# Kernel optimization log

Measured on AMD Instinct MI355X. Metric: run time of the kernel, lower is better.

Reference implementation:

```python
import jax, jax.numpy as jnp
import numpy as np

B, L, D, H = 2, 2048, 1024, 16
HD = D // H

def setup_inputs() -> dict:
    key = jax.random.key(0)
    ks = jax.random.split(key, 9)
    s = 1.0 / np.sqrt(D)
    return {
        "x": jax.random.normal(ks[0], (B, L, D), jnp.float32),
        "Wq": jax.random.normal(ks[1], (D, D), jnp.float32) * s,
        "bq": jax.random.normal(ks[2], (D,), jnp.float32) * 0.02,
        "Wk": jax.random.normal(ks[3], (D, D), jnp.float32) * s,
        "bk": jax.random.normal(ks[4], (D,), jnp.float32) * 0.02,
        "Wv": jax.random.normal(ks[5], (D, D), jnp.float32) * s,
        "bv": jax.random.normal(ks[6], (D,), jnp.float32) * 0.02,
        "Wo": jax.random.normal(ks[7], (D, D), jnp.float32) * s,
        "bo": jax.random.normal(ks[8], (D,), jnp.float32) * 0.02,
    }

def reference(x, Wq, bq, Wk, bk, Wv, bv, Wo, bo):
    b, l, d = x.shape
    # projections -> [B, H, L, HD]
    def split_heads(t):
        return t.reshape(b, l, H, HD).transpose(0, 2, 1, 3)
    Q = split_heads(x @ Wq + bq)
    K = split_heads(x @ Wk + bk)
    V = split_heads(x @ Wv + bv)
    scores = jnp.einsum('bhqd,bhkd->bhqk', Q, K)  # [B,H,L,L]
    causal = jnp.tril(jnp.ones((l, l), bool))
    scores = jnp.where(causal, scores, -jnp.inf)
    attn = jax.nn.softmax(scores / np.sqrt(HD), axis=-1)
    ctx = jnp.einsum('bhqk,bhkd->bhqd', attn, V)
    ctx = ctx.transpose(0, 2, 1, 3).reshape(b, l, d)
    return ctx @ Wo + bo
```

## Files before the change

### kernel.cpp

```cpp
#include <hip/hip_runtime.h>
#include <stdint.h>

typedef unsigned short u16;
typedef __attribute__((ext_vector_type(8))) __bf16 bf16x8;
typedef __attribute__((ext_vector_type(4))) float f32x4;
typedef __attribute__((ext_vector_type(16))) float f32x16;

#define BM 128
#define BN 128
#define BK 32

__device__ __forceinline__ u16 f2bf(float f) {
  union { float f; uint32_t u; } c; c.f = f;
  uint32_t u = c.u + 0x7fffu + ((c.u >> 16) & 1u);
  return (u16)(u >> 16);
}
__device__ __forceinline__ uint32_t cvtpk(float a, float b) {
  uint32_t r;
  asm("v_cvt_pk_bf16_f32 %0, %1, %2" : "=v"(r) : "v"(a), "v"(b));
  return r;
}

__device__ __forceinline__ void async16(const u16* g, u16* l) {
  __builtin_amdgcn_global_load_lds(
      (const __attribute__((address_space(1))) void*)g,
      (__attribute__((address_space(3))) void*)l, 16, 0, 0);
}

__device__ __forceinline__ f32x4 mfma16(bf16x8 a, bf16x8 b, f32x4 c) {
  return __builtin_amdgcn_mfma_f32_16x16x32_bf16(a, b, c, 0, 0, 0);
}
__device__ __forceinline__ f32x16 mfma32(bf16x8 a, bf16x8 b, f32x16 c) {
  return __builtin_amdgcn_mfma_f32_32x32x16_bf16(a, b, c, 0, 0, 0);
}


__global__ __launch_bounds__(256) void x_cvt_kernel(const float* __restrict__ x,
                                                    u16* __restrict__ xb) {
  int i = (blockIdx.x * 256 + threadIdx.x) * 4;
  float4 v = *(const float4*)(x + i);
  uint2 t; t.x = cvtpk(v.x, v.y); t.y = cvtpk(v.z, v.w);
  *(uint2*)(xb + i) = t;
}

__global__ __launch_bounds__(256) void wt_cvt_kernel(const float* __restrict__ Wq,
                                                     const float* __restrict__ Wk,
                                                     const float* __restrict__ Wv,
                                                     const float* __restrict__ Wo,
                                                     u16* __restrict__ out) {
  __shared__ __align__(16) u16 t[64][72];
  int z = blockIdx.z;
  const float* W = (z == 0) ? Wq : (z == 1) ? Wk : (z == 2) ? Wv : Wo;
  u16* o = out + (size_t)z * (1u << 20);
  int n0 = blockIdx.x * 64, k0 = blockIdx.y * 64;
  int tid = threadIdx.x;
  int c4 = (tid & 15) * 4, r0 = tid >> 4;
#pragma unroll
  for (int i = 0; i < 4; i++) {
    int r = r0 + i * 16;
    float4 v = *(const float4*)(W + (size_t)(k0 + r) * 1024 + n0 + c4);
    t[c4 + 0][r] = f2bf(v.x);
    t[c4 + 1][r] = f2bf(v.y);
    t[c4 + 2][r] = f2bf(v.z);
    t[c4 + 3][r] = f2bf(v.w);
  }
  __syncthreads();
  int n = tid >> 2, kc = (tid & 3) * 16;
  uint4 a = *(const uint4*)&t[n][kc];
  uint4 b = *(const uint4*)&t[n][kc + 8];
  *(uint4*)(o + (size_t)(n0 + n) * 1024 + k0 + kc) = a;
  *(uint4*)(o + (size_t)(n0 + n) * 1024 + k0 + kc + 8) = b;
}


__device__ __forceinline__ void gemm_core(const u16* __restrict__ A,
                                          const u16* __restrict__ Bt,
                                          u16* As, u16* Bs, f32x4 (&acc)[4][4]) {
  const int tid = threadIdx.x, wave = tid >> 6, lane = tid & 63;
  const int low = lane & 15, hi = lane >> 4;
  const int wm = wave >> 1, wn = wave & 1;
  const int m0 = blockIdx.y * BM, n0 = blockIdx.x * BN;
  const f32x4 fzero = {0.f, 0.f, 0.f, 0.f};
#pragma unroll
  for (int i = 0; i < 4; i++)
#pragma unroll
    for (int j = 0; j < 4; j++) acc[i][j] = fzero;

  const u16* ap = As + (wm * 64 + low) * BK + hi * 8;
  const u16* bp = Bs + (wn * 64 + low) * BK + hi * 8;

  const int e0 = wave * 128 + lane;
  const int e1 = e0 + 64;
  const u16* ga0 = A + (size_t)(m0 + (e0 >> 2)) * 1024 + (e0 & 3) * 8;
  const u16* ga1 = A + (size_t)(m0 + (e1 >> 2)) * 1024 + (e1 & 3) * 8;
  const u16* gb0 = Bt + (size_t)(n0 + (e0 >> 2)) * 1024 + (e0 & 3) * 8;
  const u16* gb1 = Bt + (size_t)(n0 + (e1 >> 2)) * 1024 + (e1 & 3) * 8;
  u16* la0 = As + (wave * 2 + 0) * 512;
  u16* la1 = As + (wave * 2 + 1) * 512;
  u16* lb0 = Bs + (wave * 2 + 0) * 512;
  u16* lb1 = Bs + (wave * 2 + 1) * 512;

  for (int kt = 0; kt < 1024; kt += BK) {
    __syncthreads();
    async16(ga0 + kt, la0);
    async16(ga1 + kt, la1);
    async16(gb0 + kt, lb0);
    async16(gb1 + kt, lb1);
    __syncthreads();
    bf16x8 af[4], bfv[4];
#pragma unroll
    for (int i = 0; i < 4; i++) af[i] = *(const bf16x8*)(ap + i * 16 * BK);
#pragma unroll
    for (int j = 0; j < 4; j++) bfv[j] = *(const bf16x8*)(bp + j * 16 * BK);
#pragma unroll
    for (int i = 0; i < 4; i++)
#pragma unroll
      for (int j = 0; j < 4; j++) acc[i][j] = mfma16(af[i], bfv[j], acc[i][j]);
  }
}

__global__ __launch_bounds__(256) void gemm_qkv_kernel(
    const u16* __restrict__ xb, const u16* __restrict__ wT,
    const float* __restrict__ bq, const float* __restrict__ bk,
    const float* __restrict__ bv,
    u16* __restrict__ qs, u16* __restrict__ ks, u16* __restrict__ vts) {
  __shared__ __align__(16) u16 As[BM * BK];
  __shared__ __align__(16) u16 Bs[BN * BK];
  const int z = blockIdx.z;
  const u16* Bt = wT + (size_t)z * (1u << 20);
  f32x4 acc[4][4];
  gemm_core(xb, Bt, As, Bs, acc);

  const float* bias = (z == 0) ? bq : (z == 1) ? bk : bv;
  u16* out = (z == 0) ? qs : (z == 1) ? ks : vts;
  const float scale = (z == 0) ? 0.180336880f : 1.0f;
  const int tid = threadIdx.x, wave = tid >> 6, lane = tid & 63;
  const int low = lane & 15, hi = lane >> 4;
  const int wm = wave >> 1, wn = wave & 1;
  const int m0 = blockIdx.y * BM, n0 = blockIdx.x * BN;
#pragma unroll
  for (int i = 0; i < 4; i++)
#pragma unroll
    for (int j = 0; j < 4; j++) {
      int gn = n0 + wn * 64 + j * 16 + low;
      float bval = bias[gn];
      int h = gn >> 6, hd = gn & 63;
#pragma unroll
      for (int r = 0; r < 4; r++) {
        int gm = m0 + wm * 64 + i * 16 + hi * 4 + r;
        int b = gm >> 11, l = gm & 2047;
        float v = (acc[i][j][r] + bval) * scale;
        size_t addr;
        if (z == 2) addr = ((size_t)((b * 16 + h) * 64 + hd)) * 2048 + l;
        else        addr = ((size_t)((b * 16 + h) * 2048 + l)) * 64 + hd;
        out[addr] = f2bf(v);
      }
    }
}

__global__ __launch_bounds__(256) void gemm_out_kernel(
    const u16* __restrict__ ctx, const u16* __restrict__ woT,
    const float* __restrict__ bo, float* __restrict__ out) {
  __shared__ __align__(16) u16 As[BM * BK];
  __shared__ __align__(16) u16 Bs[BN * BK];
  f32x4 acc[4][4];
  gemm_core(ctx, woT, As, Bs, acc);
  const int tid = threadIdx.x, wave = tid >> 6, lane = tid & 63;
  const int low = lane & 15, hi = lane >> 4;
  const int wm = wave >> 1, wn = wave & 1;
  const int m0 = blockIdx.y * BM, n0 = blockIdx.x * BN;
#pragma unroll
  for (int i = 0; i < 4; i++)
#pragma unroll
    for (int j = 0; j < 4; j++) {
      int gn = n0 + wn * 64 + j * 16 + low;
      float bval = bo[gn];
#pragma unroll
      for (int r = 0; r < 4; r++) {
        int gm = m0 + wm * 64 + i * 16 + hi * 4 + r;
        out[(size_t)gm * 1024 + gn] = acc[i][j][r] + bval;
      }
    }
}

__global__ __launch_bounds__(256) void flash_kernel(
    const u16* __restrict__ Qs, const u16* __restrict__ Ks,
    const u16* __restrict__ Vts, u16* __restrict__ ctx) {
  __shared__ __align__(16) u16 Kls[3][64 * 64];
  __shared__ __align__(16) u16 Vls[3][64 * 64];

  const int bid = blockIdx.x;
  const int qt = (bid < 256) ? (15 - (bid >> 5)) : ((bid - 256) >> 5);
  const int bh = bid & 31;
  const int qb = qt * 128;
  const int nkv = 2 * qt + 2;

  const int tid = threadIdx.x, wave = tid >> 6, lane = tid & 63;
  const int q32 = lane & 31, hi2 = lane >> 5;
  const int x7 = q32 & 7;

  const u16* Qb = Qs + (size_t)bh * (2048 * 64);
  const u16* Kb = Ks + (size_t)bh * (2048 * 64);
  const u16* Vb = Vts + (size_t)bh * (64 * 2048);

  const int qrow = qb + wave * 32 + q32;
  bf16x8 qf[4];
#pragma unroll
  for (int ds = 0; ds < 4; ds++)
    qf[ds] = *(const bf16x8*)(Qb + (size_t)qrow * 64 + ds * 16 + hi2 * 8);

  f32x16 o0, o1;
#pragma unroll
  for (int r = 0; r < 16; r++) { o0[r] = 0.f; o1[r] = 0.f; }
  float m_ = -1e30f, l_ = 0.f;

  const int srow0 = (lane >> 3);
  const int scc = lane & 7;

#define STAGE(buf, KT0)                                                        \
  {                                                                            \
    _Pragma("unroll") for (int i = 0; i < 2; i++) {                            \
      int row = (wave * 2 + i) * 8 + srow0;                                    \
      async16(Kb + (size_t)((KT0) + row) * 64 + ((scc ^ (row & 7)) * 8),       \
              &Kls[buf][(wave * 2 + i) * 512]);                                \
      async16(Vb + (size_t)row * 2048 + (KT0) + ((scc ^ (row & 7)) * 8),       \
              &Vls[buf][(wave * 2 + i) * 512]);                                \
    }                                                                          \
  }

  STAGE(0, 0)
  STAGE(1, 64)

  const int qmax = qb + wave * 32 + 31;

  int c0 = 0, c1 = 1, c2 = 2;
  for (int t = 0; t < nkv; t++) {
    const int kt0 = t * 64;
    if (t + 1 < nkv) { asm volatile("s_waitcnt vmcnt(4)" ::: "memory"); }
    else             { asm volatile("s_waitcnt vmcnt(0)" ::: "memory"); }
    __builtin_amdgcn_s_barrier();
    if (t + 2 < nkv) STAGE(c2, kt0 + 128)

    if (kt0 <= qmax) {
      const u16* Kc = &Kls[c0][0];
      const u16* Vc = &Vls[c0][0];

      f32x16 s0, s1;
#pragma unroll
      for (int r = 0; r < 16; r++) { s0[r] = 0.f; s1[r] = 0.f; }
      __builtin_amdgcn_s_setprio(1);
#pragma unroll
      for (int ds = 0; ds < 4; ds++) {
        int cc = ds * 2 + hi2;
        bf16x8 kf0 = *(const bf16x8*)(Kc + q32 * 64 + ((cc ^ x7) * 8));
        bf16x8 kf1 = *(const bf16x8*)(Kc + (32 + q32) * 64 + ((cc ^ x7) * 8));
        s0 = mfma32(kf0, qf[ds], s0);
        s1 = mfma32(kf1, qf[ds], s1);
      }
      __builtin_amdgcn_s_setprio(0);

      bf16x8 vf0[4], vf1[4];
#pragma unroll
      for (int ks = 0; ks < 4; ks++) {
        int ca = (2 * ks) ^ x7, cb = (2 * ks + 1) ^ x7;
        union { uint2 u[2]; bf16x8 v; } a, b;
        a.u[0] = *(const uint2*)(Vc + q32 * 64 + ca * 8 + 4 * hi2);
        a.u[1] = *(const uint2*)(Vc + q32 * 64 + cb * 8 + 4 * hi2);
        b.u[0] = *(const uint2*)(Vc + (32 + q32) * 64 + ca * 8 + 4 * hi2);
        b.u[1] = *(const uint2*)(Vc + (32 + q32) * 64 + cb * 8 + 4 * hi2);
        vf0[ks] = a.v; vf1[ks] = b.v;
      }

      if (kt0 + 63 > qb + wave * 32) {
#pragma unroll
        for (int r = 0; r < 16; r++) {
          int kl = (r & 3) + 8 * (r >> 2) + 4 * hi2;
          if (kt0 + kl > qrow) s0[r] = -1e30f;
          if (kt0 + 32 + kl > qrow) s1[r] = -1e30f;
        }
      }

      float pm = -1e30f;
#pragma unroll
      for (int r = 0; r < 16; r++) pm = fmaxf(pm, fmaxf(s0[r], s1[r]));
      pm = fmaxf(pm, __shfl_xor(pm, 32));
      if (__any(pm > m_ + 8.f)) {
        float mn = fmaxf(m_, pm);
        float corr = __builtin_amdgcn_exp2f(m_ - mn);
        m_ = mn;
        l_ *= corr;
#pragma unroll
        for (int r = 0; r < 16; r++) { o0[r] *= corr; o1[r] *= corr; }
      }

      float rs = 0.f;
#pragma unroll
      for (int r = 0; r < 16; r++) {
        s0[r] = __builtin_amdgcn_exp2f(s0[r] - m_);
        s1[r] = __builtin_amdgcn_exp2f(s1[r] - m_);
        rs += s0[r] + s1[r];
      }
      rs += __shfl_xor(rs, 32);
      l_ += rs;

      bf16x8 pb[4];
#pragma unroll
      for (int ks = 0; ks < 4; ks++) {
        union { uint32_t u[4]; bf16x8 v; } pu;
        if (ks < 2) {
          int rb = 8 * ks;
          pu.u[0] = cvtpk(s0[rb + 0], s0[rb + 1]);
          pu.u[1] = cvtpk(s0[rb + 2], s0[rb + 3]);
          pu.u[2] = cvtpk(s0[rb + 4], s0[rb + 5]);
          pu.u[3] = cvtpk(s0[rb + 6], s0[rb + 7]);
        } else {
          int rb = 8 * (ks - 2);
          pu.u[0] = cvtpk(s1[rb + 0], s1[rb + 1]);
          pu.u[1] = cvtpk(s1[rb + 2], s1[rb + 3]);
          pu.u[2] = cvtpk(s1[rb + 4], s1[rb + 5]);
          pu.u[3] = cvtpk(s1[rb + 6], s1[rb + 7]);
        }
        pb[ks] = pu.v;
      }

      __builtin_amdgcn_s_setprio(1);
#pragma unroll
      for (int ks = 0; ks < 4; ks++) {
        o0 = mfma32(vf0[ks], pb[ks], o0);
        o1 = mfma32(vf1[ks], pb[ks], o1);
      }
      __builtin_amdgcn_s_setprio(0);
    }

    int tmp = c0; c0 = c1; c1 = c2; c2 = tmp;
  }

  const int b = bh >> 4, h = bh & 15;
  float inv = 1.f / l_;
  size_t base = ((size_t)(b * 2048 + qrow)) * 1024 + h * 64;
#pragma unroll
  for (int m = 0; m < 4; m++) {
    uint2 w0, w1;
    w0.x = cvtpk(o0[4 * m + 0] * inv, o0[4 * m + 1] * inv);
    w0.y = cvtpk(o0[4 * m + 2] * inv, o0[4 * m + 3] * inv);
    *(uint2*)(ctx + base + 8 * m + 4 * hi2) = w0;
    w1.x = cvtpk(o1[4 * m + 0] * inv, o1[4 * m + 1] * inv);
    w1.y = cvtpk(o1[4 * m + 2] * inv, o1[4 * m + 3] * inv);
    *(uint2*)(ctx + base + 32 + 8 * m + 4 * hi2) = w1;
  }
}


extern "C" void kernel_launch(void* const* d_in, const int* in_sizes, int n_in,
                              void* d_out, int out_size, void* d_ws, size_t ws_size,
                              hipStream_t stream) {
  const float* x  = (const float*)d_in[0];
  const float* Wq = (const float*)d_in[1];
  const float* bq = (const float*)d_in[2];
  const float* Wk = (const float*)d_in[3];
  const float* bk = (const float*)d_in[4];
  const float* Wv = (const float*)d_in[5];
  const float* bv = (const float*)d_in[6];
  const float* Wo = (const float*)d_in[7];
  const float* bo = (const float*)d_in[8];

  char* ws = (char*)d_ws;
  u16* xb  = (u16*)(ws);
  u16* wT  = (u16*)(ws + (8u << 20));
  u16* qs  = (u16*)(ws + (16u << 20));
  u16* ks  = (u16*)(ws + (24u << 20));
  u16* vts = (u16*)(ws + (32u << 20));
  u16* ctx = (u16*)(ws + (40u << 20));

  x_cvt_kernel<<<4096, 256, 0, stream>>>(x, xb);
  wt_cvt_kernel<<<dim3(16, 16, 4), 256, 0, stream>>>(Wq, Wk, Wv, Wo, wT);
  gemm_qkv_kernel<<<dim3(8, 32, 3), 256, 0, stream>>>(xb, wT, bq, bk, bv, qs, ks, vts);
  flash_kernel<<<512, 256, 0, stream>>>(qs, ks, vts, ctx);
  gemm_out_kernel<<<dim3(8, 32), 256, 0, stream>>>(ctx, wT + 3 * (1u << 20), bo, (float*)d_out);
}
```

Baseline: 130.9 us.

## Use 128-wide KV tiles with double buffering and permuted V layout in flash kernel

The flash attention kernel now processes 128 keys per iteration instead of 64, switching from triple-buffered 64-row tiles to double-buffered 128-row tiles. This halves the number of barriers and softmax rescale passes per query tile. The V projection output is stored with a permutation of sequence-index bits 2 and 3, so each V fragment can be read from LDS as one 16-byte load instead of two 8-byte loads. In exchange, the prefetch is only one tile deep with a full vmcnt(0) wait, which can expose load latency. Register pressure also rises from holding four score accumulators.

Result: slower. 137.2 us (+4.8%).

```diff
diff --git a/kernel.cpp b/kernel.cpp
--- a/kernel.cpp
+++ b/kernel.cpp
@@ -151,8 +151,12 @@
         int b = gm >> 11, l = gm & 2047;
         float v = (acc[i][j][r] + bval) * scale;
         size_t addr;
-        if (z == 2) addr = ((size_t)((b * 16 + h) * 64 + hd)) * 2048 + l;
-        else        addr = ((size_t)((b * 16 + h) * 2048 + l)) * 64 + hd;
+        if (z == 2) {
+          int lp = (l & ~12) | ((l & 4) << 1) | ((l & 8) >> 1);
+          addr = ((size_t)((b * 16 + h) * 64 + hd)) * 2048 + lp;
+        } else {
+          addr = ((size_t)((b * 16 + h) * 2048 + l)) * 64 + hd;
+        }
         out[addr] = f2bf(v);
       }
     }
@@ -186,14 +190,14 @@
 __global__ __launch_bounds__(256) void flash_kernel(
     const u16* __restrict__ Qs, const u16* __restrict__ Ks,
     const u16* __restrict__ Vts, u16* __restrict__ ctx) {
-  __shared__ __align__(16) u16 Kls[3][64 * 64];
-  __shared__ __align__(16) u16 Vls[3][64 * 64];
+  __shared__ __align__(16) u16 Kls[2][128 * 64];
+  __shared__ __align__(16) u16 Vls[2][64 * 128];
 
   const int bid = blockIdx.x;
   const int qt = (bid < 256) ? (15 - (bid >> 5)) : ((bid - 256) >> 5);
   const int bh = bid & 31;
   const int qb = qt * 128;
-  const int nkv = 2 * qt + 2;
+  const int nt = qt + 1;
 
   const int tid = threadIdx.x, wave = tid >> 6, lane = tid & 63;
   const int q32 = lane & 31, hi2 = lane >> 5;
@@ -209,130 +213,177 @@
   for (int ds = 0; ds < 4; ds++)
     qf[ds] = *(const bf16x8*)(Qb + (size_t)qrow * 64 + ds * 16 + hi2 * 8);
 
-  f32x16 o0, o1;
-#pragma unroll
-  for (int r = 0; r < 16; r++) { o0[r] = 0.f; o1[r] = 0.f; }
+  f32x16 o0, o1, z16;
+#pragma unroll
+  for (int r = 0; r < 16; r++) { o0[r] = 0.f; o1[r] = 0.f; z16[r] = 0.f; }
   float m_ = -1e30f, l_ = 0.f;
 
-  const int srow0 = (lane >> 3);
-  const int scc = lane & 7;
+  const int kslc = wave * 4;
 
 #define STAGE(buf, KT0)                                                        \
   {                                                                            \
-    _Pragma("unroll") for (int i = 0; i < 2; i++) {                            \
-      int row = (wave * 2 + i) * 8 + srow0;                                    \
-      async16(Kb + (size_t)((KT0) + row) * 64 + ((scc ^ (row & 7)) * 8),       \
-              &Kls[buf][(wave * 2 + i) * 512]);                                \
-      async16(Vb + (size_t)row * 2048 + (KT0) + ((scc ^ (row & 7)) * 8),       \
-              &Vls[buf][(wave * 2 + i) * 512]);                                \
+    _Pragma("unroll") for (int i = 0; i < 4; i++) {                            \
+      int krow = (kslc + i) * 8 + (lane >> 3);                                 \
+      async16(Kb + (size_t)((KT0) + krow) * 64 +                               \
+                  (((lane & 7) ^ (krow & 7)) * 8),                             \
+              &Kls[buf][(kslc + i) * 512]);                                    \
+      int vrow = (kslc + i) * 4 + (lane >> 4);                                 \
+      int oc = (lane & 8) | ((lane & 7) ^ (vrow & 7));                         \
+      async16(Vb + (size_t)vrow * 2048 + (KT0) + oc * 8,                       \
+              &Vls[buf][(kslc + i) * 512]);                                    \
     }                                                                          \
   }
 
   STAGE(0, 0)
-  STAGE(1, 64)
 
   const int qmax = qb + wave * 32 + 31;
-
-  int c0 = 0, c1 = 1, c2 = 2;
-  for (int t = 0; t < nkv; t++) {
-    const int kt0 = t * 64;
-    if (t + 1 < nkv) { asm volatile("s_waitcnt vmcnt(4)" ::: "memory"); }
-    else             { asm volatile("s_waitcnt vmcnt(0)" ::: "memory"); }
+  int cur = 0;
+  for (int t = 0; t < nt; t++) {
+    const int kt0 = t * 128;
+    asm volatile("s_waitcnt vmcnt(0)" ::: "memory");
     __builtin_amdgcn_s_barrier();
-    if (t + 2 < nkv) STAGE(c2, kt0 + 128)
-
-    if (kt0 <= qmax) {
-      const u16* Kc = &Kls[c0][0];
-      const u16* Vc = &Vls[c0][0];
-
-      f32x16 s0, s1;
-#pragma unroll
-      for (int r = 0; r < 16; r++) { s0[r] = 0.f; s1[r] = 0.f; }
-      __builtin_amdgcn_s_setprio(1);
+    if (t + 1 < nt) STAGE(cur ^ 1, kt0 + 128)
+
+    const u16* Kc = &Kls[cur][0];
+    const u16* Vc = &Vls[cur][0];
+    const bool full = (kt0 + 64 <= qmax);
+
+    f32x16 s0, s1, s2, s3;
+    __builtin_amdgcn_s_setprio(1);
+#pragma unroll
+    for (int ds = 0; ds < 4; ds++) {
+      int cs = ((ds * 2 + hi2) ^ x7) * 8;
+      bf16x8 kf0 = *(const bf16x8*)(Kc + q32 * 64 + cs);
+      bf16x8 kf1 = *(const bf16x8*)(Kc + (32 + q32) * 64 + cs);
+      s0 = mfma32(kf0, qf[ds], ds ? s0 : z16);
+      s1 = mfma32(kf1, qf[ds], ds ? s1 : z16);
+    }
+    if (full) {
 #pragma unroll
       for (int ds = 0; ds < 4; ds++) {
-        int cc = ds * 2 + hi2;
-        bf16x8 kf0 = *(const bf16x8*)(Kc + q32 * 64 + ((cc ^ x7) * 8));
-        bf16x8 kf1 = *(const bf16x8*)(Kc + (32 + q32) * 64 + ((cc ^ x7) * 8));
-        s0 = mfma32(kf0, qf[ds], s0);
-        s1 = mfma32(kf1, qf[ds], s1);
-      }
-      __builtin_amdgcn_s_setprio(0);
-
-      bf16x8 vf0[4], vf1[4];
-#pragma unroll
-      for (int ks = 0; ks < 4; ks++) {
-        int ca = (2 * ks) ^ x7, cb = (2 * ks + 1) ^ x7;
-        union { uint2 u[2]; bf16x8 v; } a, b;
-        a.u[0] = *(const uint2*)(Vc + q32 * 64 + ca * 8 + 4 * hi2);
-        a.u[1] = *(const uint2*)(Vc + q32 * 64 + cb * 8 + 4 * hi2);
-        b.u[0] = *(const uint2*)(Vc + (32 + q32) * 64 + ca * 8 + 4 * hi2);
-        b.u[1] = *(const uint2*)(Vc + (32 + q32) * 64 + cb * 8 + 4 * hi2);
-        vf0[ks] = a.v; vf1[ks] = b.v;
-      }
-
-      if (kt0 + 63 > qb + wave * 32) {
+        int cs = ((ds * 2 + hi2) ^ x7) * 8;
+        bf16x8 kf2 = *(const bf16x8*)(Kc + (64 + q32) * 64 + cs);
+        bf16x8 kf3 = *(const bf16x8*)(Kc + (96 + q32) * 64 + cs);
+        s2 = mfma32(kf2, qf[ds], ds ? s2 : z16);
+        s3 = mfma32(kf3, qf[ds], ds ? s3 : z16);
+      }
+    }
+    __builtin_amdgcn_s_setprio(0);
+
+    bf16x8 vA0[4], vA1[4];
+#pragma unroll
+    for (int ksx = 0; ksx < 4; ksx++) {
+      int sc = ((2 * ksx + hi2) ^ x7) * 8;
+      vA0[ksx] = *(const bf16x8*)(Vc + q32 * 128 + sc);
+      vA1[ksx] = *(const bf16x8*)(Vc + (32 + q32) * 128 + sc);
+    }
+
+    if (kt0 + 127 > qb + wave * 32) {
+#pragma unroll
+      for (int r = 0; r < 16; r++) {
+        int kl = (r & 3) + 8 * (r >> 2) + 4 * hi2;
+        if (kt0 + kl > qrow) s0[r] = -1e30f;
+        if (kt0 + 32 + kl > qrow) s1[r] = -1e30f;
+      }
+      if (full) {
 #pragma unroll
         for (int r = 0; r < 16; r++) {
           int kl = (r & 3) + 8 * (r >> 2) + 4 * hi2;
-          if (kt0 + kl > qrow) s0[r] = -1e30f;
-          if (kt0 + 32 + kl > qrow) s1[r] = -1e30f;
+          if (kt0 + 64 + kl > qrow) s2[r] = -1e30f;
+          if (kt0 + 96 + kl > qrow) s3[r] = -1e30f;
         }
       }
-
-      float pm = -1e30f;
-#pragma unroll
-      for (int r = 0; r < 16; r++) pm = fmaxf(pm, fmaxf(s0[r], s1[r]));
-      pm = fmaxf(pm, __shfl_xor(pm, 32));
-      if (__any(pm > m_ + 8.f)) {
-        float mn = fmaxf(m_, pm);
-        float corr = __builtin_amdgcn_exp2f(m_ - mn);
-        m_ = mn;
-        l_ *= corr;
-#pragma unroll
-        for (int r = 0; r < 16; r++) { o0[r] *= corr; o1[r] *= corr; }
-      }
-
-      float rs = 0.f;
+    }
+
+    float pm = -1e30f;
+#pragma unroll
+    for (int r = 0; r < 16; r++) pm = fmaxf(pm, fmaxf(s0[r], s1[r]));
+    if (full) {
+#pragma unroll
+      for (int r = 0; r < 16; r++) pm = fmaxf(pm, fmaxf(s2[r], s3[r]));
+    }
+    pm = fmaxf(pm, __shfl_xor(pm, 32));
+    if (__any(pm > m_ + 8.f)) {
+      float mn = fmaxf(m_, pm);
+      float corr = __builtin_amdgcn_exp2f(m_ - mn);
+      m_ = mn;
+      l_ *= corr;
+#pragma unroll
+      for (int r = 0; r < 16; r++) { o0[r] *= corr; o1[r] *= corr; }
+    }
+
+    float rs = 0.f;
+#pragma unroll
+    for (int r = 0; r < 16; r++) {
+      s0[r] = __builtin_amdgcn_exp2f(s0[r] - m_);
+      s1[r] = __builtin_amdgcn_exp2f(s1[r] - m_);
+      rs += s0[r] + s1[r];
+    }
+    if (full) {
 #pragma unroll
       for (int r = 0; r < 16; r++) {
-        s0[r] = __builtin_amdgcn_exp2f(s0[r] - m_);
-        s1[r] = __builtin_amdgcn_exp2f(s1[r] - m_);
-        rs += s0[r] + s1[r];
-      }
-      rs += __shfl_xor(rs, 32);
-      l_ += rs;
-
-      bf16x8 pb[4];
-#pragma unroll
-      for (int ks = 0; ks < 4; ks++) {
+        s2[r] = __builtin_amdgcn_exp2f(s2[r] - m_);
+        s3[r] = __builtin_amdgcn_exp2f(s3[r] - m_);
+        rs += s2[r] + s3[r];
+      }
+    }
+    rs += __shfl_xor(rs, 32);
+    l_ += rs;
+
+    __builtin_amdgcn_s_setprio(1);
+#pragma unroll
+    for (int ksx = 0; ksx < 4; ksx++) {
+      union { uint32_t u[4]; bf16x8 v; } pu;
+      if (ksx < 2) {
+        int rb = 8 * ksx;
+        pu.u[0] = cvtpk(s0[rb + 0], s0[rb + 1]);
+        pu.u[1] = cvtpk(s0[rb + 2], s0[rb + 3]);
+        pu.u[2] = cvtpk(s0[rb + 4], s0[rb + 5]);
+        pu.u[3] = cvtpk(s0[rb + 6], s0[rb + 7]);
+      } else {
+        int rb = 8 * (ksx - 2);
+        pu.u[0] = cvtpk(s1[rb + 0], s1[rb + 1]);
+        pu.u[1] = cvtpk(s1[rb + 2], s1[rb + 3]);
+        pu.u[2] = cvtpk(s1[rb + 4], s1[rb + 5]);
+        pu.u[3] = cvtpk(s1[rb + 6], s1[rb + 7]);
+      }
+      o0 = mfma32(vA0[ksx], pu.v, o0);
+      o1 = mfma32(vA1[ksx], pu.v, o1);
+    }
+    __builtin_amdgcn_s_setprio(0);
+
+    if (full) {
+      bf16x8 vB0[4], vB1[4];
+#pragma unroll
+      for (int ksx = 0; ksx < 4; ksx++) {
+        int sc = (8 + ((2 * ksx + hi2) ^ x7)) * 8;
+        vB0[ksx] = *(const bf16x8*)(Vc + q32 * 128 + sc);
+        vB1[ksx] = *(const bf16x8*)(Vc + (32 + q32) * 128 + sc);
+      }
+      __builtin_amdgcn_s_setprio(1);
+#pragma unroll
+      for (int ksx = 0; ksx < 4; ksx++) {
         union { uint32_t u[4]; bf16x8 v; } pu;
-        if (ks < 2) {
-          int rb = 8 * ks;
-          pu.u[0] = cvtpk(s0[rb + 0], s0[rb + 1]);
-          pu.u[1] = cvtpk(s0[rb + 2], s0[rb + 3]);
-          pu.u[2] = cvtpk(s0[rb + 4], s0[rb + 5]);
-          pu.u[3] = cvtpk(s0[rb + 6], s0[rb + 7]);
+        if (ksx < 2) {
+          int rb = 8 * ksx;
+          pu.u[0] = cvtpk(s2[rb + 0], s2[rb + 1]);
+          pu.u[1] = cvtpk(s2[rb + 2], s2[rb + 3]);
+          pu.u[2] = cvtpk(s2[rb + 4], s2[rb + 5]);
+          pu.u[3] = cvtpk(s2[rb + 6], s2[rb + 7]);
         } else {
-          int rb = 8 * (ks - 2);
-          pu.u[0] = cvtpk(s1[rb + 0], s1[rb + 1]);
-          pu.u[1] = cvtpk(s1[rb + 2], s1[rb + 3]);
-          pu.u[2] = cvtpk(s1[rb + 4], s1[rb + 5]);
-          pu.u[3] = cvtpk(s1[rb + 6], s1[rb + 7]);
+          int rb = 8 * (ksx - 2);
+          pu.u[0] = cvtpk(s3[rb + 0], s3[rb + 1]);
+          pu.u[1] = cvtpk(s3[rb + 2], s3[rb + 3]);
+          pu.u[2] = cvtpk(s3[rb + 4], s3[rb + 5]);
+          pu.u[3] = cvtpk(s3[rb + 6], s3[rb + 7]);
         }
-        pb[ks] = pu.v;
-      }
-
-      __builtin_amdgcn_s_setprio(1);
-#pragma unroll
-      for (int ks = 0; ks < 4; ks++) {
-        o0 = mfma32(vf0[ks], pb[ks], o0);
-        o1 = mfma32(vf1[ks], pb[ks], o1);
+        o0 = mfma32(vB0[ksx], pu.v, o0);
+        o1 = mfma32(vB1[ksx], pu.v, o1);
       }
       __builtin_amdgcn_s_setprio(0);
     }
 
-    int tmp = c0; c0 = c1; c1 = c2; c2 = tmp;
+    cur ^= 1;
   }
 
   const int b = bh >> 4, h = bh & 15;
```

## Double-buffer GEMM loads, shrink output GEMM tile, permute V layout for wide reads

Applied to the files above, without the earlier changes.

The shared GEMM core now double-buffers its LDS tiles, so the next K-slice's async global-to-LDS copies are issued while MFMAs run on the current slice. This drops one barrier per iteration. The output projection uses 128x64 tiles with twice as many blocks, which gives better CU occupancy on the 256-tile grid. The V^T store permutes sequence positions within groups of 16, so the flash kernel can load V fragments with single 16-byte LDS reads instead of paired 8-byte reads. The cost is double the LDS use in the GEMMs and a layout coupling between the QKV epilogue and the attention kernel.

Measured after the change: 132.3 us. About the same (+1.1%).

```diff
diff --git a/kernel.cpp b/kernel.cpp
--- a/kernel.cpp
+++ b/kernel.cpp
@@ -5,10 +5,6 @@
 typedef __attribute__((ext_vector_type(8))) __bf16 bf16x8;
 typedef __attribute__((ext_vector_type(4))) float f32x4;
 typedef __attribute__((ext_vector_type(16))) float f32x16;
-
-#define BM 128
-#define BN 128
-#define BK 32
 
 __device__ __forceinline__ u16 f2bf(float f) {
   union { float f; uint32_t u; } c; c.f = f;
@@ -72,51 +68,67 @@
   *(uint4*)(o + (size_t)(n0 + n) * 1024 + k0 + kc + 8) = b;
 }
 
-
-__device__ __forceinline__ void gemm_core(const u16* __restrict__ A,
-                                          const u16* __restrict__ Bt,
-                                          u16* As, u16* Bs, f32x4 (&acc)[4][4]) {
+template <int TN>
+__device__ __forceinline__ void gemm_core2(const u16* __restrict__ A,
+                                           const u16* __restrict__ Bt,
+                                           u16* As, u16* Bs,
+                                           f32x4 (&acc)[4][TN / 32]) {
+  constexpr int NJ = TN / 32;
+  constexpr int ASZ = 128 * 32, BSZ = TN * 32;
   const int tid = threadIdx.x, wave = tid >> 6, lane = tid & 63;
   const int low = lane & 15, hi = lane >> 4;
   const int wm = wave >> 1, wn = wave & 1;
-  const int m0 = blockIdx.y * BM, n0 = blockIdx.x * BN;
+  const int m0 = blockIdx.y * 128, n0 = blockIdx.x * TN;
   const f32x4 fzero = {0.f, 0.f, 0.f, 0.f};
 #pragma unroll
   for (int i = 0; i < 4; i++)
 #pragma unroll
-    for (int j = 0; j < 4; j++) acc[i][j] = fzero;
-
-  const u16* ap = As + (wm * 64 + low) * BK + hi * 8;
-  const u16* bp = Bs + (wn * 64 + low) * BK + hi * 8;
-
-  const int e0 = wave * 128 + lane;
-  const int e1 = e0 + 64;
-  const u16* ga0 = A + (size_t)(m0 + (e0 >> 2)) * 1024 + (e0 & 3) * 8;
-  const u16* ga1 = A + (size_t)(m0 + (e1 >> 2)) * 1024 + (e1 & 3) * 8;
-  const u16* gb0 = Bt + (size_t)(n0 + (e0 >> 2)) * 1024 + (e0 & 3) * 8;
-  const u16* gb1 = Bt + (size_t)(n0 + (e1 >> 2)) * 1024 + (e1 & 3) * 8;
+    for (int j = 0; j < NJ; j++) acc[i][j] = fzero;
+
+  const int ea0 = wave * 128 + lane, ea1 = ea0 + 64;
+  const u16* ga0 = A + (size_t)(m0 + (ea0 >> 2)) * 1024 + (ea0 & 3) * 8;
+  const u16* ga1 = A + (size_t)(m0 + (ea1 >> 2)) * 1024 + (ea1 & 3) * 8;
   u16* la0 = As + (wave * 2 + 0) * 512;
   u16* la1 = As + (wave * 2 + 1) * 512;
-  u16* lb0 = Bs + (wave * 2 + 0) * 512;
+
+  const int eb0 = (TN == 128) ? (wave * 128 + lane) : (wave * 64 + lane);
+  const int eb1 = eb0 + 64;
+  const u16* gb0 = Bt + (size_t)(n0 + (eb0 >> 2)) * 1024 + (eb0 & 3) * 8;
+  const u16* gb1 = Bt + (size_t)(n0 + (eb1 >> 2)) * 1024 + (eb1 & 3) * 8;
+  u16* lb0 = Bs + ((TN == 128) ? (wave * 2 + 0) * 512 : wave * 512);
   u16* lb1 = Bs + (wave * 2 + 1) * 512;
 
-  for (int kt = 0; kt < 1024; kt += BK) {
+  const u16* ap = As + (wm * 64 + low) * 32 + hi * 8;
+  const u16* bp = Bs + (wn * (TN / 2) + low) * 32 + hi * 8;
+
+#define GSTAGE(buf, KT)                                                        \
+  {                                                                            \
+    async16(ga0 + (KT), la0 + (buf) * ASZ);                                    \
+    async16(ga1 + (KT), la1 + (buf) * ASZ);                                    \
+    async16(gb0 + (KT), lb0 + (buf) * BSZ);                                    \
+    if (TN == 128) async16(gb1 + (KT), lb1 + (buf) * BSZ);                     \
+  }
+
+  GSTAGE(0, 0)
+  __syncthreads();
+  int buf = 0;
+  for (int kt = 0; kt < 1024; kt += 32) {
+    if (kt + 32 < 1024) GSTAGE(buf ^ 1, kt + 32)
+    bf16x8 af[4], bfv[NJ];
+#pragma unroll
+    for (int i = 0; i < 4; i++)
+      af[i] = *(const bf16x8*)(ap + buf * ASZ + i * 16 * 32);
+#pragma unroll
+    for (int j = 0; j < NJ; j++)
+      bfv[j] = *(const bf16x8*)(bp + buf * BSZ + j * 16 * 32);
+#pragma unroll
+    for (int i = 0; i < 4; i++)
+#pragma unroll
+      for (int j = 0; j < NJ; j++) acc[i][j] = mfma16(af[i], bfv[j], acc[i][j]);
     __syncthreads();
-    async16(ga0 + kt, la0);
-    async16(ga1 + kt, la1);
-    async16(gb0 + kt, lb0);
-    async16(gb1 + kt, lb1);
-    __syncthreads();
-    bf16x8 af[4], bfv[4];
-#pragma unroll
-    for (int i = 0; i < 4; i++) af[i] = *(const bf16x8*)(ap + i * 16 * BK);
-#pragma unroll
-    for (int j = 0; j < 4; j++) bfv[j] = *(const bf16x8*)(bp + j * 16 * BK);
-#pragma unroll
-    for (int i = 0; i < 4; i++)
-#pragma unroll
-      for (int j = 0; j < 4; j++) acc[i][j] = mfma16(af[i], bfv[j], acc[i][j]);
-  }
+    buf ^= 1;
+  }
+#undef GSTAGE
 }
 
 __global__ __launch_bounds__(256) void gemm_qkv_kernel(
@@ -124,12 +136,12 @@
     const float* __restrict__ bq, const float* __restrict__ bk,
     const float* __restrict__ bv,
     u16* __restrict__ qs, u16* __restrict__ ks, u16* __restrict__ vts) {
-  __shared__ __align__(16) u16 As[BM * BK];
-  __shared__ __align__(16) u16 Bs[BN * BK];
+  __shared__ __align__(16) u16 As[2 * 128 * 32];
+  __shared__ __align__(16) u16 Bs[2 * 128 * 32];
   const int z = blockIdx.z;
   const u16* Bt = wT + (size_t)z * (1u << 20);
   f32x4 acc[4][4];
-  gemm_core(xb, Bt, As, Bs, acc);
+  gemm_core2<128>(xb, Bt, As, Bs, acc);
 
   const float* bias = (z == 0) ? bq : (z == 1) ? bk : bv;
   u16* out = (z == 0) ? qs : (z == 1) ? ks : vts;
@@ -137,7 +149,7 @@
   const int tid = threadIdx.x, wave = tid >> 6, lane = tid & 63;
   const int low = lane & 15, hi = lane >> 4;
   const int wm = wave >> 1, wn = wave & 1;
-  const int m0 = blockIdx.y * BM, n0 = blockIdx.x * BN;
+  const int m0 = blockIdx.y * 128, n0 = blockIdx.x * 128;
 #pragma unroll
   for (int i = 0; i < 4; i++)
 #pragma unroll
@@ -151,8 +163,12 @@
         int b = gm >> 11, l = gm & 2047;
         float v = (acc[i][j][r] + bval) * scale;
         size_t addr;
-        if (z == 2) addr = ((size_t)((b * 16 + h) * 64 + hd)) * 2048 + l;
-        else        addr = ((size_t)((b * 16 + h) * 2048 + l)) * 64 + hd;
+        if (z == 2) {
+          int lp = (l & ~12) | ((l & 4) << 1) | ((l & 8) >> 1);
+          addr = ((size_t)((b * 16 + h) * 64 + hd)) * 2048 + lp;
+        } else {
+          addr = ((size_t)((b * 16 + h) * 2048 + l)) * 64 + hd;
+        }
         out[addr] = f2bf(v);
       }
     }
@@ -161,19 +177,19 @@
 __global__ __launch_bounds__(256) void gemm_out_kernel(
     const u16* __restrict__ ctx, const u16* __restrict__ woT,
     const float* __restrict__ bo, float* __restrict__ out) {
-  __shared__ __align__(16) u16 As[BM * BK];
-  __shared__ __align__(16) u16 Bs[BN * BK];
-  f32x4 acc[4][4];
-  gemm_core(ctx, woT, As, Bs, acc);
+  __shared__ __align__(16) u16 As[2 * 128 * 32];
+  __shared__ __align__(16) u16 Bs[2 * 64 * 32];
+  f32x4 acc[4][2];
+  gemm_core2<64>(ctx, woT, As, Bs, acc);
   const int tid = threadIdx.x, wave = tid >> 6, lane = tid & 63;
   const int low = lane & 15, hi = lane >> 4;
   const int wm = wave >> 1, wn = wave & 1;
-  const int m0 = blockIdx.y * BM, n0 = blockIdx.x * BN;
+  const int m0 = blockIdx.y * 128, n0 = blockIdx.x * 64;
 #pragma unroll
   for (int i = 0; i < 4; i++)
 #pragma unroll
-    for (int j = 0; j < 4; j++) {
-      int gn = n0 + wn * 64 + j * 16 + low;
+    for (int j = 0; j < 2; j++) {
+      int gn = n0 + wn * 32 + j * 16 + low;
       float bval = bo[gn];
 #pragma unroll
       for (int r = 0; r < 4; r++) {
@@ -251,9 +267,9 @@
       __builtin_amdgcn_s_setprio(1);
 #pragma unroll
       for (int ds = 0; ds < 4; ds++) {
-        int cc = ds * 2 + hi2;
-        bf16x8 kf0 = *(const bf16x8*)(Kc + q32 * 64 + ((cc ^ x7) * 8));
-        bf16x8 kf1 = *(const bf16x8*)(Kc + (32 + q32) * 64 + ((cc ^ x7) * 8));
+        int cs = ((ds * 2 + hi2) ^ x7) * 8;
+        bf16x8 kf0 = *(const bf16x8*)(Kc + q32 * 64 + cs);
+        bf16x8 kf1 = *(const bf16x8*)(Kc + (32 + q32) * 64 + cs);
         s0 = mfma32(kf0, qf[ds], s0);
         s1 = mfma32(kf1, qf[ds], s1);
       }
@@ -261,14 +277,10 @@
 
       bf16x8 vf0[4], vf1[4];
 #pragma unroll
-      for (int ks = 0; ks < 4; ks++) {
-        int ca = (2 * ks) ^ x7, cb = (2 * ks + 1) ^ x7;
-        union { uint2 u[2]; bf16x8 v; } a, b;
-        a.u[0] = *(const uint2*)(Vc + q32 * 64 + ca * 8 + 4 * hi2);
-        a.u[1] = *(const uint2*)(Vc + q32 * 64 + cb * 8 + 4 * hi2);
-        b.u[0] = *(const uint2*)(Vc + (32 + q32) * 64 + ca * 8 + 4 * hi2);
-        b.u[1] = *(const uint2*)(Vc + (32 + q32) * 64 + cb * 8 + 4 * hi2);
-        vf0[ks] = a.v; vf1[ks] = b.v;
+      for (int ksx = 0; ksx < 4; ksx++) {
+        int sc = ((2 * ksx + hi2) ^ x7) * 8;
+        vf0[ksx] = *(const bf16x8*)(Vc + q32 * 64 + sc);
+        vf1[ksx] = *(const bf16x8*)(Vc + (32 + q32) * 64 + sc);
       }
 
       if (kt0 + 63 > qb + wave * 32) {
@@ -305,29 +317,29 @@
 
       bf16x8 pb[4];
 #pragma unroll
-      for (int ks = 0; ks < 4; ks++) {
+      for (int ksx = 0; ksx < 4; ksx++) {
         union { uint32_t u[4]; bf16x8 v; } pu;
-        if (ks < 2) {
-          int rb = 8 * ks;
+        if (ksx < 2) {
+          int rb = 8 * ksx;
           pu.u[0] = cvtpk(s0[rb + 0], s0[rb + 1]);
           pu.u[1] = cvtpk(s0[rb + 2], s0[rb + 3]);
           pu.u[2] = cvtpk(s0[rb + 4], s0[rb + 5]);
           pu.u[3] = cvtpk(s0[rb + 6], s0[rb + 7]);
         } else {
-          int rb = 8 * (ks - 2);
+          int rb = 8 * (ksx - 2);
           pu.u[0] = cvtpk(s1[rb + 0], s1[rb + 1]);
           pu.u[1] = cvtpk(s1[rb + 2], s1[rb + 3]);
           pu.u[2] = cvtpk(s1[rb + 4], s1[rb + 5]);
           pu.u[3] = cvtpk(s1[rb + 6], s1[rb + 7]);
         }
-        pb[ks] = pu.v;
+        pb[ksx] = pu.v;
       }
 
       __builtin_amdgcn_s_setprio(1);
 #pragma unroll
-      for (int ks = 0; ks < 4; ks++) {
-        o0 = mfma32(vf0[ks], pb[ks], o0);
-        o1 = mfma32(vf1[ks], pb[ks], o1);
+      for (int ksx = 0; ksx < 4; ksx++) {
+        o0 = mfma32(vf0[ksx], pb[ksx], o0);
+        o1 = mfma32(vf1[ksx], pb[ksx], o1);
       }
       __builtin_amdgcn_s_setprio(0);
     }
@@ -376,5 +388,5 @@
   wt_cvt_kernel<<<dim3(16, 16, 4), 256, 0, stream>>>(Wq, Wk, Wv, Wo, wT);
   gemm_qkv_kernel<<<dim3(8, 32, 3), 256, 0, stream>>>(xb, wT, bq, bk, bv, qs, ks, vts);
   flash_kernel<<<512, 256, 0, stream>>>(qs, ks, vts, ctx);
-  gemm_out_kernel<<<dim3(8, 32), 256, 0, stream>>>(ctx, wT + 3 * (1u << 20), bo, (float*)d_out);
-}
+  gemm_out_kernel<<<dim3(16, 32), 256, 0, stream>>>(ctx, wT + 3 * (1u << 20), bo, (float*)d_out);
+}
```
